# Kernel optimization log

Measured on AMD Instinct MI355X. Metric: run time of the kernel, lower is better.

Reference implementation:

```python
import jax, jax.numpy as jnp
import numpy as np

EPS = 1e-8

def _cosine_rows(a, b):
    na = jnp.maximum(jnp.linalg.norm(a, axis=1), EPS)
    nb = jnp.maximum(jnp.linalg.norm(b, axis=1), EPS)
    return jnp.sum(a * b, axis=1) / (na * nb)


def setup_inputs() -> dict:
    key = jax.random.key(0)
    k1, k2 = jax.random.split(key)
    X = jax.random.normal(k1, (16384, 1024), dtype=jnp.float32)
    dictionary = jax.random.normal(k2, (4096, 1024), dtype=jnp.float32)
    descriptors = jnp.arange(4096, dtype=jnp.int64)
    return {"X": X, "dictionary": dictionary, "descriptors": descriptors, "k": 16}


def reference(X, dictionary, descriptors, k):
    # SOMP with centering=True, criterion='l1', pc=None (default forward path)
    orig_X = X
    std_orig_sum = jnp.sum(jnp.var(orig_X, axis=0, ddof=1))
    X_mean = jnp.mean(X, axis=0, keepdims=True)   # [1, D]
    Xc = X - X_mean                               # centered data [N, D]

    M = dictionary.shape[0]
    notchosen = jnp.ones((M,), dtype=X.dtype)
    residual = Xc
    chosen, evr, l2, cosine = [], [], [], []
    W = None
    recon = jnp.zeros_like(Xc)

    for i in range(k):  # k is a static Python int -> unrolled, per-step shapes static
        cross = residual @ dictionary.T           # [N, M] -- dominant memory traffic
        scores = jnp.sum(jnp.abs(cross * notchosen), axis=0)  # l1 criterion
        idx = jnp.argmax(scores)
        chosen.append(idx)
        notchosen = notchosen.at[idx].set(0)

        atoms = dictionary[jnp.stack(chosen)]     # [i+1, D], dynamic gather, static shape
        # least squares: min ||atoms.T @ W - Xc.T||  (full column rank -> normal eqs)
        G = atoms @ atoms.T                       # [i+1, i+1]
        W = jnp.linalg.solve(G, atoms @ Xc.T)     # [i+1, N]
        recon = (atoms.T @ W).T                   # [N, D]
        residual = Xc - recon

        rec_full = X_mean + recon
        evr.append(jnp.sum(jnp.var(rec_full, axis=0, ddof=1)) / std_orig_sum)
        cosine.append(jnp.mean(_cosine_rows(orig_X, rec_full)))
        l2.append(jnp.mean((orig_X - rec_full) ** 2))

    weights = jnp.linalg.norm(W, axis=1)          # [k]
    chosen_arr = jnp.stack(chosen)
    recon_out = X_mean + recon
    residual_out = Xc - recon                     # == X - recon_out
    return (recon_out, residual_out, chosen_arr, weights, W.T,
            jnp.stack(evr), jnp.stack(l2), jnp.stack(cosine))
```

## Files before the change

### kernel.cpp

```cpp
#include <hip/hip_runtime.h>
#include <math.h>

#define NROWS 16384
#define DIMK  1024
#define MDIC  4096
#define KSEL  16

#define OFF_RECON   0
#define OFF_RESID   ((size_t)NROWS*DIMK)
#define OFF_CHOSEN  ((size_t)2*NROWS*DIMK)
#define OFF_WEIGHTS (OFF_CHOSEN + 16)
#define OFF_WT      (OFF_WEIGHTS + 16)
#define OFF_EVR     (OFF_WT + (size_t)NROWS*KSEL)
#define OFF_L2      (OFF_EVR + 16)
#define OFF_COS     (OFF_L2 + 16)

typedef unsigned short u16;
typedef unsigned long long u64;
typedef __attribute__((ext_vector_type(8))) short short8;
typedef __attribute__((ext_vector_type(4))) float f32x4;

__device__ inline float blockReduce256f(float v) {
    __shared__ float ws_[4];
    #pragma unroll
    for (int off = 32; off > 0; off >>= 1) v += __shfl_down(v, off);
    __syncthreads();
    if ((threadIdx.x & 63) == 0) ws_[threadIdx.x >> 6] = v;
    __syncthreads();
    return ws_[0] + ws_[1] + ws_[2] + ws_[3];
}

__device__ inline void wredStore(double v, int k, int lane, int wv, double (*accS)[4]) {
    #pragma unroll
    for (int off = 32; off > 0; off >>= 1) v += __shfl_down(v, off);
    if (lane == 0) accS[k][wv] = v;
}

__device__ inline u16 f2bf(float f) {
    unsigned u = __float_as_uint(f);
    unsigned r = u + 0x7FFFu + ((u >> 16) & 1u);
    return (u16)(r >> 16);
}
__device__ inline float bf2f(u16 h) { return __uint_as_float(((unsigned)h) << 16); }

__global__ void k_init(float* notchosen, u64* amx, u64* statsAcc, u64* ctr2) {
    int m = blockIdx.x * 256 + threadIdx.x;
    if (m < MDIC) notchosen[m] = 1.0f;
    if (blockIdx.x == 0) {
        if (threadIdx.x < 40) statsAcc[threadIdx.x] = 0ULL;
        if (threadIdx.x < 2)  amx[threadIdx.x] = 0ULL;
        if (threadIdx.x == 0) *ctr2 = 0ULL;
    }
}

__global__ __launch_bounds__(256) void k_colstats(const float* __restrict__ X,
                                                  float* __restrict__ colpart,
                                                  float* __restrict__ sqpart) {
    int d  = blockIdx.x * 256 + threadIdx.x;
    int r0 = blockIdx.y * 256;
    float s = 0.f, sq = 0.f;
    for (int r = 0; r < 256; ++r) {
        float v = X[(size_t)(r0 + r) * DIMK + d];
        s += v; sq += v * v;
    }
    colpart[(size_t)blockIdx.y * DIMK + d] = s;
    __shared__ float red[256];
    red[threadIdx.x] = sq; __syncthreads();
    for (int off = 128; off > 0; off >>= 1) {
        if (threadIdx.x < off) red[threadIdx.x] += red[threadIdx.x + off];
        __syncthreads();
    }
    if (threadIdx.x == 0) sqpart[blockIdx.y * 4 + blockIdx.x] = red[0];
}

__global__ __launch_bounds__(1024) void k_reduce_mean(const float* __restrict__ colpart,
                                                      const float* __restrict__ sqpart,
                                                      float* __restrict__ xmean,
                                                      double* __restrict__ scal) {
    int d = threadIdx.x;
    double s = 0.0;
    for (int y = 0; y < 64; ++y) s += (double)colpart[(size_t)y * DIMK + d];
    float m = (float)(s / (double)NROWS);
    xmean[d] = m;
    __shared__ double red[1024];
    red[d] = (double)m * (double)m; __syncthreads();
    for (int off = 512; off > 0; off >>= 1) {
        if (d < off) red[d] += red[d + off];
        __syncthreads();
    }
    if (d == 0) {
        double xmn2 = red[0];
        double sx2 = 0.0;
        for (int i = 0; i < 256; ++i) sx2 += (double)sqpart[i];
        scal[0] = sx2;
        scal[1] = sx2 - (double)NROWS * xmn2;
        scal[2] = xmn2;
    }
}

__global__ __launch_bounds__(256) void k_md(const float* __restrict__ Dict,
                                            const float* __restrict__ xmean,
                                            float* __restrict__ md,
                                            float* __restrict__ Dnorm2) {
    int m = blockIdx.x, t = threadIdx.x;
    float4 a = ((const float4*)(Dict + (size_t)m * DIMK))[t];
    float4 b = ((const float4*)xmean)[t];
    float s  = a.x * b.x + a.y * b.y + a.z * b.z + a.w * b.w;
    float sn = a.x * a.x + a.y * a.y + a.z * a.z + a.w * a.w;
    s  = blockReduce256f(s);
    sn = blockReduce256f(sn);
    if (t == 0) { md[m] = s; Dnorm2[m] = sn; }
}

__global__ __launch_bounds__(256) void k_split(const float* __restrict__ src,
                                               u16* __restrict__ hi,
                                               u16* __restrict__ lo) {
    size_t idx = ((size_t)blockIdx.x * 256 + threadIdx.x) * 4;
    float4 v = *(const float4*)(src + idx);
    ushort4 h, l;
    h.x = f2bf(v.x); l.x = f2bf(v.x - bf2f(h.x));
    h.y = f2bf(v.y); l.y = f2bf(v.y - bf2f(h.y));
    h.z = f2bf(v.z); l.z = f2bf(v.z - bf2f(h.z));
    h.w = f2bf(v.w); l.w = f2bf(v.w - bf2f(h.w));
    *(ushort4*)(hi + idx) = h;
    *(ushort4*)(lo + idx) = l;
}

__global__ __launch_bounds__(256) void k_splitX(const float* __restrict__ src,
                                                u16* __restrict__ hi,
                                                u16* __restrict__ lo,
                                                const float* __restrict__ xmean,
                                                float* __restrict__ Xnorm2,
                                                float* __restrict__ XdotM) {
    int n = blockIdx.x, t = threadIdx.x;
    size_t idx = (size_t)n * DIMK + t * 4;
    float4 v = *(const float4*)(src + idx);
    float4 mv = ((const float4*)xmean)[t];
    ushort4 h, l;
    h.x = f2bf(v.x); l.x = f2bf(v.x - bf2f(h.x));
    h.y = f2bf(v.y); l.y = f2bf(v.y - bf2f(h.y));
    h.z = f2bf(v.z); l.z = f2bf(v.z - bf2f(h.z));
    h.w = f2bf(v.w); l.w = f2bf(v.w - bf2f(h.w));
    *(ushort4*)(hi + idx) = h;
    *(ushort4*)(lo + idx) = l;
    float s2 = v.x * v.x + v.y * v.y + v.z * v.z + v.w * v.w;
    float sm = v.x * mv.x + v.y * mv.y + v.z * mv.z + v.w * mv.w;
    s2 = blockReduce256f(s2);
    sm = blockReduce256f(sm);
    if (t == 0) { Xnorm2[n] = s2; XdotM[n] = sm; }
}


#define GLL16(g, l) __builtin_amdgcn_global_load_lds( \
    (__attribute__((address_space(1))) void*)(g), \
    (__attribute__((address_space(3))) void*)(l), 16, 0, 0)

#define STAGE_A2(pa_, kc_, wb_, q0_, q1_) do { \
    GLL16((pa_) + aGbase + (size_t)(q0_) * 64 * DIMK + (kc_), \
          sA + (wb_) * 16384 + (q0_) * 4096 + lWbase); \
    GLL16((pa_) + aGbase + (size_t)(q1_) * 64 * DIMK + (kc_), \
          sA + (wb_) * 16384 + (q1_) * 4096 + lWbase); \
} while (0)

#define STAGE_B2(pb_, kc_, wb_, q0_, q1_) do { \
    GLL16((pb_) + bGbase + (size_t)(q0_) * 64 * DIMK + (kc_), \
          sB + (wb_) * 16384 + (q0_) * 4096 + lWbase); \
    GLL16((pb_) + bGbase + (size_t)(q1_) * 64 * DIMK + (kc_), \
          sB + (wb_) * 16384 + (q1_) * 4096 + lWbase); \
} while (0)

#define VM4 asm volatile("s_waitcnt vmcnt(4)" ::: "memory")
#define VM2 asm volatile("s_waitcnt vmcnt(2)" ::: "memory")
#define VM0 asm volatile("s_waitcnt vmcnt(0)" ::: "memory")
#define NOPSTMT ((void)0)

#define PHASE(rb_, mq_, nq_, STAGE_STMT, WAIT_STMT) do { \
    short8 af[4][2], bfv[2][2]; \
    const u16* pA_ = sA + (rb_) * 16384; \
    const u16* pB_ = sB + (rb_) * 16384; \
    _Pragma("unroll") \
    for (int fi = 0; fi < 4; ++fi) { \
        af[fi][0] = *(const short8*)&pA_[aoffA0 + ((mq_) * 4 + fi) * 1024]; \
        af[fi][1] = *(const short8*)&pA_[aoffA1 + ((mq_) * 4 + fi) * 1024]; \
    } \
    _Pragma("unroll") \
    for (int fj = 0; fj < 2; ++fj) { \
        bfv[fj][0] = *(const short8*)&pB_[boffB0 + ((nq_) * 2 + fj) * 1024]; \
        bfv[fj][1] = *(const short8*)&pB_[boffB1 + ((nq_) * 2 + fj) * 1024]; \
    } \
    STAGE_STMT; \
    __builtin_amdgcn_s_barrier(); \
    __builtin_amdgcn_s_setprio(1); \
    _Pragma("unroll") \
    for (int fi = 0; fi < 4; ++fi) \
        _Pragma("unroll") \
        for (int fj = 0; fj < 2; ++fj) { \
            acc[(mq_) * 4 + fi][(nq_) * 2 + fj] = __builtin_amdgcn_mfma_f32_16x16x32_bf16( \
                af[fi][0], bfv[fj][0], acc[(mq_) * 4 + fi][(nq_) * 2 + fj], 0, 0, 0); \
            acc[(mq_) * 4 + fi][(nq_) * 2 + fj] = __builtin_amdgcn_mfma_f32_16x16x32_bf16( \
                af[fi][1], bfv[fj][1], acc[(mq_) * 4 + fi][(nq_) * 2 + fj], 0, 0, 0); \
        } \
    __builtin_amdgcn_s_setprio(0); \
    WAIT_STMT; \
    __builtin_amdgcn_s_barrier(); \
} while (0)

__global__ __launch_bounds__(512, 2) void k_gemm8(const u16* __restrict__ Ahi,
                                                  const u16* __restrict__ Alo,
                                                  const u16* __restrict__ Bhi,
                                                  const u16* __restrict__ Blo,
                                                  const float* __restrict__ md,
                                                  u16* __restrict__ C0h,
                                                  int rowAbase) {
    __shared__ u16 sA[2 * 16384];
    __shared__ u16 sB[2 * 16384];
    int T = threadIdx.x;
    int lane = T & 63, wid = T >> 6;
    int wr = wid >> 2, wc = wid & 3;

    int nwg = gridDim.x, cpx = nwg >> 3;
    int bid = blockIdx.x;
    int wg  = (bid & 7) * cpx + (bid >> 3);
    int bm = wg >> 4, bn = wg & 15;
    int rowA0 = bm * 256, rowB0 = bn * 256;

    int sw = (T & 7) ^ ((T >> 3) & 7);
    size_t aGbase = (size_t)(rowA0 + (T >> 3)) * DIMK + sw * 8;
    size_t bGbase = (size_t)(rowB0 + (T >> 3)) * DIMK + sw * 8;
    int lWbase = (T >> 6) * 512;

    int lm = lane & 15, lk = lane >> 4;
    int kb0 = (lk * 16) ^ ((lane & 7) << 4);
    int kb1 = (64 + lk * 16) ^ ((lane & 7) << 4);
    int aoffA0 = (wr * 128 + lm) * 64 + (kb0 >> 1);
    int aoffA1 = (wr * 128 + lm) * 64 + (kb1 >> 1);
    int boffB0 = (wc * 64 + lm) * 64 + (kb0 >> 1);
    int boffB1 = (wc * 64 + lm) * 64 + (kb1 >> 1);

    f32x4 acc[8][4];
    f32x4 zero = {0.f, 0.f, 0.f, 0.f};
    #pragma unroll
    for (int i = 0; i < 8; ++i)
        #pragma unroll
        for (int j = 0; j < 4; ++j) acc[i][j] = zero;

    STAGE_B2(Bhi, 0, 0, 0, 1);
    STAGE_B2(Bhi, 0, 0, 2, 3);
    STAGE_A2(Ahi, 0, 0, 0, 2);
    STAGE_A2(Ahi, 0, 0, 1, 3);
    VM2;
    __builtin_amdgcn_s_barrier();

    for (int t = 0; t < 47; ++t) {
        int rbuf = t & 1, wbuf = rbuf ^ 1;
        int kk = (t + 1) << 6;
        int seg = kk >> 10;
        const u16* pa = (seg == 1) ? Alo : Ahi;
        const u16* pb = (seg == 2) ? Blo : Bhi;
        int kc = kk & 1023;
        PHASE(rbuf, 0, 0, STAGE_B2(pb, kc, wbuf, 0, 1), NOPSTMT);
        PHASE(rbuf, 0, 1, STAGE_B2(pb, kc, wbuf, 2, 3), VM4);
        PHASE(rbuf, 1, 0, STAGE_A2(pa, kc, wbuf, 0, 2), NOPSTMT);
        PHASE(rbuf, 1, 1, STAGE_A2(pa, kc, wbuf, 1, 3), VM2);
    }
    PHASE(1, 0, 0, NOPSTMT, NOPSTMT);
    PHASE(1, 0, 1, NOPSTMT, VM0);
    PHASE(1, 1, 0, NOPSTMT, NOPSTMT);
    PHASE(1, 1, 1, NOPSTMT, NOPSTMT);

    #pragma unroll
    for (int nf = 0; nf < 4; ++nf) {
        int m = rowB0 + wc * 64 + nf * 16 + lm;
        float mdv = md[m];
        #pragma unroll
        for (int mf = 0; mf < 8; ++mf) {
            int nb = rowAbase + rowA0 + wr * 128 + mf * 16 + lk * 4;
            #pragma unroll
            for (int r = 0; r < 4; ++r)
                C0h[(size_t)(nb + r) * MDIC + m] = f2bf(acc[mf][nf][r] - mdv);
        }
    }
}

template <int NA>
__global__ __launch_bounds__(256) void k_score(const u16* __restrict__ C0h,
                                               const float* __restrict__ GR,
                                               const float* __restrict__ Wm,
                                               float* __restrict__ scorePf) {
    constexpr int NAX = NA ? NA : 1;
    __shared__ float Wl[NAX][64];
    int t = threadIdx.x;
    int m0 = blockIdx.x * 1024 + t * 4;
    int n0 = blockIdx.y * 64;
    float4 gr[NAX];
    #pragma unroll
    for (int j = 0; j < NA; ++j) gr[j] = *(const float4*)&GR[(size_t)j * MDIC + m0];
    for (int idx = t; idx < NA * 64; idx += 256) {
        int j = idx >> 6, nn = idx & 63;
        Wl[j][nn] = Wm[(size_t)j * NROWS + n0 + nn];
    }
    __syncthreads();
    float4 acc = {0.f, 0.f, 0.f, 0.f};
    for (int nn = 0; nn < 64; ++nn) {
        ushort4 ch = *(const ushort4*)&C0h[(size_t)(n0 + nn) * MDIC + m0];
        float4 c = {bf2f(ch.x), bf2f(ch.y), bf2f(ch.z), bf2f(ch.w)};
        float4 cr = {0.f, 0.f, 0.f, 0.f};
        #pragma unroll
        for (int j = 0; j < NA; ++j) {
            float wv = Wl[j][nn];
            cr.x += wv * gr[j].x; cr.y += wv * gr[j].y;
            cr.z += wv * gr[j].z; cr.w += wv * gr[j].w;
        }
        acc.x += fabsf(c.x - cr.x); acc.y += fabsf(c.y - cr.y);
        acc.z += fabsf(c.z - cr.z); acc.w += fabsf(c.w - cr.w);
    }
    *(float4*)&scorePf[(size_t)blockIdx.y * MDIC + m0] = acc;
}

__global__ __launch_bounds__(256) void k_scoreargmax(const float* __restrict__ scorePf,
                                                     float* __restrict__ notchosen,
                                                     u64* __restrict__ amx,
                                                     int* __restrict__ chosen,
                                                     float* __restrict__ outChosen,
                                                     const float* __restrict__ md,
                                                     const float* __restrict__ Dnorm2,
                                                     const float* __restrict__ GR,
                                                     float* __restrict__ Lmat,
                                                     float* __restrict__ Gcc,
                                                     float* __restrict__ mdot,
                                                     int iter) {
    int t = threadIdx.x;
    int m0 = blockIdx.x * 256;
    int tm = t & 63, yg = t >> 6;
    float sx = 0.f, sy = 0.f, sz = 0.f, sw = 0.f;
    #pragma unroll 4
    for (int y = yg; y < 256; y += 4) {
        float4 v = *(const float4*)&scorePf[(size_t)y * MDIC + m0 + (tm << 2)];
        sx += v.x; sy += v.y; sz += v.z; sw += v.w;
    }
    __shared__ float4 red4[4][64];
    float4 pv; pv.x = sx; pv.y = sy; pv.z = sz; pv.w = sw;
    red4[yg][tm] = pv;
    __syncthreads();
    u64 best = 0ULL;
    if (t < 64) {
        float4 a = red4[0][t], b = red4[1][t], cc = red4[2][t], d = red4[3][t];
        double sv[4] = {(double)a.x + b.x + cc.x + d.x,
                        (double)a.y + b.y + cc.y + d.y,
                        (double)a.z + b.z + cc.z + d.z,
                        (double)a.w + b.w + cc.w + d.w};
        int mb = m0 + (t << 2);
        #pragma unroll
        for (int j = 0; j < 4; ++j) {
            if (notchosen[mb + j] != 0.f) {
                u64 key = ((u64)__double_as_longlong(sv[j]) & ~0xFFFULL) | (u64)(4095 - (mb + j));
                if (key > best) best = key;
            }
        }
        #pragma unroll
        for (int off = 32; off > 0; off >>= 1) {
            u64 o = __shfl_down(best, off);
            if (o > best) best = o;
        }
    }
    __shared__ int slast, sc;
    if (t == 0) {
        atomicMax(&amx[0], best);
        __threadfence();
        u64 done = atomicAdd(&amx[1], 1ULL);
        slast = (done == 15ULL) ? 1 : 0;
        if (slast) {
            u64 k = atomicMax(&amx[0], 0ULL);
            int c = 4095 - (int)(k & 0xFFFULL);
            sc = c;
            chosen[iter] = c;
            notchosen[c] = 0.f;
            outChosen[iter] = (float)c;
            mdot[iter] = md[c];
            amx[0] = 0ULL; amx[1] = 0ULL;
        }
    }
    __syncthreads();
    if (!slast) return;
    int c = sc;
    __shared__ float Lsh[16][16];
    __shared__ float g[17];
    __shared__ float LrowS[16];
    Lsh[t >> 4][t & 15] = Lmat[t];
    if (t < iter)  g[t] = GR[(size_t)t * MDIC + c];
    if (t == iter) g[t] = Dnorm2[c];
    __syncthreads();
    if (t == 0) {
        for (int b = 0; b < iter; ++b) {
            float s = g[b];
            for (int x = 0; x < b; ++x) s -= LrowS[x] * Lsh[b][x];
            LrowS[b] = s / Lsh[b][b];
        }
        float s2 = g[iter];
        for (int x = 0; x < iter; ++x) s2 -= LrowS[x] * LrowS[x];
        LrowS[iter] = sqrtf(fmaxf(s2, 1e-20f));
        for (int b = 0; b <= iter; ++b) Lmat[iter * 16 + b] = LrowS[b];
        for (int b = iter + 1; b < 16; ++b) Lmat[iter * 16 + b] = 0.f;
        for (int b = 0; b < iter; ++b) { Gcc[iter * 16 + b] = g[b]; Gcc[b * 16 + iter] = g[b]; }
        Gcc[iter * 16 + iter] = g[iter];
    }
}

template <int NAT>
__global__ __launch_bounds__(256) void k_gramsolve(const float* __restrict__ Dict,
                                                   const int* __restrict__ chosen,
                                                   const u16* __restrict__ C0h,
                                                   float* __restrict__ GR,
                                                   float* __restrict__ Bm,
                                                   const float* __restrict__ Lmat,
                                                   const float* __restrict__ Gcc_g,
                                                   const float* __restrict__ mdot,
                                                   const float* __restrict__ Xnorm2,
                                                   const float* __restrict__ XdotM,
                                                   const double* __restrict__ scal,
                                                   float* __restrict__ Wm,
                                                   u64* __restrict__ statsAcc,
                                                   u64* __restrict__ ctr2,
                                                   float* __restrict__ out, int iter) {
    int t = threadIdx.x;
    int c = chosen[iter];
    if (blockIdx.x >= 64) {
        int m = blockIdx.x - 64;
        float4 a = ((const float4*)(Dict + (size_t)c * DIMK))[t];
        float4 b = ((const float4*)(Dict + (size_t)m * DIMK))[t];
        float s = a.x * b.x + a.y * b.y + a.z * b.z + a.w * b.w;
        s = blockReduce256f(s);
        if (t == 0) GR[(size_t)iter * MDIC + m] = s;
        return;
    }
    constexpr int NV = 3 + 2 * NAT;
    __shared__ float L[16][16];
    __shared__ float G[16][16];
    __shared__ float mdl[16];
    __shared__ double accS[35][4];
    if (t < NAT * NAT) {
        int a = t / NAT, b2 = t % NAT;
        L[a][b2] = Lmat[a * 16 + b2];
        G[a][b2] = Gcc_g[a * 16 + b2];
    }
    if (t < NAT) mdl[t] = mdot[t];
    __syncthreads();
    int n = blockIdx.x * 256 + t;
    float b[NAT], y[NAT], w[NAT];
    #pragma unroll
    for (int j = 0; j < NAT - 1; ++j) b[j] = Bm[(size_t)j * NROWS + n];
    float bn = bf2f(C0h[(size_t)n * MDIC + c]);
    b[NAT - 1] = bn;
    Bm[(size_t)(NAT - 1) * NROWS + n] = bn;
    #pragma unroll
    for (int a = 0; a < NAT; ++a) {
        float s = b[a];
        #pragma unroll
        for (int x = 0; x < NAT; ++x) if (x < a) s -= L[a][x] * y[x];
        y[a] = s / L[a][a];
    }
    #pragma unroll
    for (int a = NAT - 1; a >= 0; --a) {
        float s = y[a];
        #pragma unroll
        for (int x = 0; x < NAT; ++x) if (x > a) s -= L[x][a] * w[x];
        w[a] = s / L[a][a];
    }
    #pragma unroll
    for (int j = 0; j < NAT; ++j) Wm[(size_t)j * NROWS + n] = w[j];

    float q = 0.f, wb = 0.f, wmd = 0.f, num1 = 0.f;
    #pragma unroll
    for (int j = 0; j < NAT; ++j) {
        float gw = 0.f;
        #pragma unroll
        for (int x = 0; x < NAT; ++x) gw += G[j][x] * w[x];
        q    += w[j] * gw;
        wb   += w[j] * b[j];
        wmd  += w[j] * mdl[j];
        num1 += w[j] * (b[j] + mdl[j]);
    }
    float xmn2 = (float)scal[2];
    float rec2 = xmn2 + 2.f * wmd + q;
    float na = fmaxf(sqrtf(Xnorm2[n]), 1e-8f);
    float nb = fmaxf(sqrtf(fmaxf(rec2, 0.f)), 1e-8f);
    float cosn = (XdotM[n] + num1) / (na * nb);

    int lane = t & 63, wv = t >> 6;
    wredStore((double)q,    0, lane, wv, accS);
    wredStore((double)wb,   1, lane, wv, accS);
    wredStore((double)cosn, 2, lane, wv, accS);
    #pragma unroll
    for (int j = 0; j < NAT; ++j) {
        wredStore((double)w[j],                 3 + j,       lane, wv, accS);
        wredStore((double)w[j] * (double)w[j],  3 + NAT + j, lane, wv, accS);
    }
    __syncthreads();
    if (t < NV) {
        double tot = accS[t][0] + accS[t][1] + accS[t][2] + accS[t][3];
        long long fx = (long long)(tot * 1048576.0);
        atomicAdd(&statsAcc[t], (u64)fx);
    }
    __shared__ int slast2;
    __syncthreads();
    if (t == 0) {
        __threadfence();
        slast2 = (atomicAdd(ctr2, 1ULL) == 63ULL) ? 1 : 0;
    }
    __syncthreads();
    if (!slast2) return;
    __shared__ double stot[35];
    __shared__ double wbarS[16];
    if (t < NV) {
        u64 raw = atomicAdd(&statsAcc[t], 0ULL);
        stot[t] = (double)(long long)raw * (1.0 / 1048576.0);
        statsAcc[t] = 0ULL;
    }
    if (t == 0) *ctr2 = 0ULL;
    __syncthreads();
    if (t < NAT) wbarS[t] = stot[3 + t] * (1.0 / (double)NROWS);
    __syncthreads();
    if (t == 0) {
        double q2 = stot[0], wb2 = stot[1], cs = stot[2];
        double wg = 0.0;
        for (int a = 0; a < NAT; ++a)
            for (int b2 = 0; b2 < NAT; ++b2) wg += wbarS[a] * wbarS[b2] * (double)G[a][b2];
        double sumXc2 = scal[1];
        out[OFF_EVR + iter] = (float)((q2 - (double)NROWS * wg) / sumXc2);
        out[OFF_L2  + iter] = (float)((sumXc2 - 2.0 * wb2 + q2) / ((double)NROWS * (double)DIMK));
        out[OFF_COS + iter] = (float)(cs / (double)NROWS);
        if (NAT == KSEL) {
            for (int j = 0; j < NAT; ++j)
                out[OFF_WEIGHTS + j] = (float)sqrt(stot[3 + NAT + j]);
        }
    }
}

__global__ __launch_bounds__(256) void k_outfinal(const float* __restrict__ X,
                                                  const float* __restrict__ xmean,
                                                  const float* __restrict__ Dict,
                                                  const int* __restrict__ chosen,
                                                  const float* __restrict__ Wm,
                                                  float* __restrict__ out) {
    __shared__ int cI[16];
    int t = threadIdx.x;
    if (t < 16) cI[t] = chosen[t];
    __syncthreads();
    int n0 = blockIdx.x * 8;
    if (t < 128) {
        int j = t & 15, r = t >> 4;
        int n = n0 + r;
        out[OFF_WT + (size_t)n * 16 + j] = Wm[(size_t)j * NROWS + n];
    }
    float4 xm = ((const float4*)xmean)[t];
    for (int r = 0; r < 8; ++r) {
        int n = n0 + r;
        float w[16];
        #pragma unroll
        for (int j = 0; j < 16; ++j) w[j] = Wm[(size_t)j * NROWS + n];
        float4 rec = xm;
        #pragma unroll
        for (int j = 0; j < 16; ++j) {
            float4 a = ((const float4*)(Dict + (size_t)cI[j] * DIMK))[t];
            rec.x += w[j] * a.x; rec.y += w[j] * a.y;
            rec.z += w[j] * a.z; rec.w += w[j] * a.w;
        }
        float4 xv = ((const float4*)(X + (size_t)n * DIMK))[t];
        float4 res = {xv.x - rec.x, xv.y - rec.y, xv.z - rec.z, xv.w - rec.w};
        ((float4*)(out + OFF_RECON + (size_t)n * DIMK))[t] = rec;
        ((float4*)(out + OFF_RESID + (size_t)n * DIMK))[t] = res;
    }
}

struct IterArgs {
    const float *X, *Dict;
    u16 *C0h;
    float *GR, *W, *Bm, *md, *Dnorm2, *xmean, *Xnorm2, *XdotM, *notchosen, *Lmat, *Gcc, *mdot;
    float *scorePf;
    u64 *amx, *statsAcc, *ctr2;
    double *scal;
    int *chosen;
    float *out;
    hipStream_t stream;
};

template <int I>
static void run_iter(const IterArgs& a) {
    k_score<I><<<dim3(4, 256), 256, 0, a.stream>>>(a.C0h, a.GR, a.W, a.scorePf);
    k_scoreargmax<<<16, 256, 0, a.stream>>>(a.scorePf, a.notchosen, a.amx, a.chosen,
                                            a.out + OFF_CHOSEN, a.md, a.Dnorm2, a.GR,
                                            a.Lmat, a.Gcc, a.mdot, I);
    k_gramsolve<I + 1><<<MDIC + 64, 256, 0, a.stream>>>(a.Dict, a.chosen, a.C0h, a.GR,
                                                        a.Bm, a.Lmat, a.Gcc, a.mdot,
                                                        a.Xnorm2, a.XdotM, a.scal, a.W,
                                                        a.statsAcc, a.ctr2, a.out, I);
}

template <int I>
struct Loop {
    static void go(const IterArgs& a) { run_iter<I>(a); Loop<I + 1>::go(a); }
};
template <>
struct Loop<KSEL> { static void go(const IterArgs&) {} };

extern "C" void kernel_launch(void* const* d_in, const int* in_sizes, int n_in,
                              void* d_out, int out_size, void* d_ws, size_t ws_size,
                              hipStream_t stream) {
    (void)in_sizes; (void)n_in; (void)out_size;
    const float* X    = (const float*)d_in[0];
    const float* Dict = (const float*)d_in[1];
    float* out = (float*)d_out;

    char* ws = (char*)d_ws;
    size_t off = 0;
    auto carve = [&](size_t bytes) -> char* {
        char* p = ws + off;
        off += (bytes + 255) & ~(size_t)255;
        return p;
    };
    u16*    C0h       = (u16*)   carve((size_t)NROWS * MDIC * 2);
    float*  GR        = (float*) carve((size_t)KSEL * MDIC * 4);
    float*  W         = (float*) carve((size_t)KSEL * NROWS * 4);
    float*  Bm        = (float*) carve((size_t)KSEL * NROWS * 4);
    float*  md        = (float*) carve((size_t)MDIC * 4);
    float*  Dnorm2    = (float*) carve((size_t)MDIC * 4);
    float*  xmean     = (float*) carve((size_t)DIMK * 4);
    float*  colpart   = (float*) carve((size_t)64 * DIMK * 4);
    float*  sqpart    = (float*) carve(256 * 4);
    float*  Xnorm2    = (float*) carve((size_t)NROWS * 4);
    float*  XdotM     = (float*) carve((size_t)NROWS * 4);
    float*  scorePf   = (float*) carve((size_t)256 * MDIC * 4);
    float*  notchosen = (float*) carve((size_t)MDIC * 4);
    u64*    amx       = (u64*)   carve(2 * 8);
    u64*    statsAcc  = (u64*)   carve(40 * 8);
    u64*    ctr2      = (u64*)   carve(8);
    int*    chosen    = (int*)   carve(KSEL * 4);
    float*  Lmat      = (float*) carve(256 * 4);
    float*  Gcc       = (float*) carve(256 * 4);
    float*  mdot      = (float*) carve(16 * 4);
    double* scal      = (double*)carve(8 * 8);
    u16*    Bhi       = (u16*)   carve((size_t)MDIC * DIMK * 2);
    u16*    Blo       = (u16*)   carve((size_t)MDIC * DIMK * 2);

    int chunkrows = 0;
    for (int cr = NROWS; cr >= 256; cr >>= 1) {
        size_t need = (size_t)cr * DIMK * 2 * 2 + 512;
        if (off + need <= ws_size) { chunkrows = cr; break; }
    }
    if (chunkrows == 0) chunkrows = 256;
    u16* Ahi = (u16*) carve((size_t)chunkrows * DIMK * 2);
    u16* Alo = (u16*) carve((size_t)chunkrows * DIMK * 2);

    k_init<<<MDIC / 256, 256, 0, stream>>>(notchosen, amx, statsAcc, ctr2);
    k_colstats<<<dim3(4, 64), 256, 0, stream>>>(X, colpart, sqpart);
    k_reduce_mean<<<1, 1024, 0, stream>>>(colpart, sqpart, xmean, scal);
    k_md<<<MDIC, 256, 0, stream>>>(Dict, xmean, md, Dnorm2);

    k_split<<<(MDIC * DIMK) / 1024, 256, 0, stream>>>(Dict, Bhi, Blo);
    int nchunks = NROWS / chunkrows;
    for (int c = 0; c < nchunks; ++c) {
        k_splitX<<<chunkrows, 256, 0, stream>>>(
            X + (size_t)c * chunkrows * DIMK, Ahi, Alo, xmean,
            Xnorm2 + (size_t)c * chunkrows, XdotM + (size_t)c * chunkrows);
        int mtiles = chunkrows / 256;
        k_gemm8<<<dim3(mtiles * 16), 512, 0, stream>>>(
            Ahi, Alo, Bhi, Blo, md, C0h, c * chunkrows);
    }

    IterArgs a{X, Dict, C0h, GR, W, Bm, md, Dnorm2, xmean, Xnorm2, XdotM, notchosen,
               Lmat, Gcc, mdot, scorePf, amx, statsAcc, ctr2, scal, chosen, out, stream};
    Loop<0>::go(a);

    k_outfinal<<<NROWS / 8, 256, 0, stream>>>(X, xmean, Dict, chosen, W, out);
}
```

Measured before the change: 1.524 ms.

## Reorder GEMM inner phases by k-half to reuse B fragments across phases

The four per-tile phases of the bf16 MFMA GEMM are reorganised. Each phase now covers one k-half for a 4x4 block of accumulators instead of a 4x2 block over the full k slice. B fragments loaded in the first phase of each k-half are kept in registers and reused by the next phase, which loads only A. This halves the LDS fragment reads per tile. The global-load wait moves from the second phase to the first, which may expose more memory latency, and the extra live fragment registers could raise register pressure.

```diff
diff --git a/kernel.cpp b/kernel.cpp
--- a/kernel.cpp
+++ b/kernel.cpp
@@ -169,37 +169,49 @@
           sB + (wb_) * 16384 + (q1_) * 4096 + lWbase); \
 } while (0)
 
-#define VM4 asm volatile("s_waitcnt vmcnt(4)" ::: "memory")
 #define VM2 asm volatile("s_waitcnt vmcnt(2)" ::: "memory")
 #define VM0 asm volatile("s_waitcnt vmcnt(0)" ::: "memory")
 #define NOPSTMT ((void)0)
 
-#define PHASE(rb_, mq_, nq_, STAGE_STMT, WAIT_STMT) do { \
-    short8 af[4][2], bfv[2][2]; \
+#define PHASE_BA(rb_, s_, STAGE_STMT, WAIT_STMT) do { \
     const u16* pA_ = sA + (rb_) * 16384; \
     const u16* pB_ = sB + (rb_) * 16384; \
+    int ko_ = (s_) ? koff1 : koff0; \
     _Pragma("unroll") \
-    for (int fi = 0; fi < 4; ++fi) { \
-        af[fi][0] = *(const short8*)&pA_[aoffA0 + ((mq_) * 4 + fi) * 1024]; \
-        af[fi][1] = *(const short8*)&pA_[aoffA1 + ((mq_) * 4 + fi) * 1024]; \
-    } \
+    for (int nf = 0; nf < 4; ++nf) \
+        bq[nf] = *(const short8*)&pB_[boffB + nf * 1024 + ko_]; \
     _Pragma("unroll") \
-    for (int fj = 0; fj < 2; ++fj) { \
-        bfv[fj][0] = *(const short8*)&pB_[boffB0 + ((nq_) * 2 + fj) * 1024]; \
-        bfv[fj][1] = *(const short8*)&pB_[boffB1 + ((nq_) * 2 + fj) * 1024]; \
-    } \
+    for (int fi = 0; fi < 4; ++fi) \
+        aq[fi] = *(const short8*)&pA_[aoffA + fi * 1024 + ko_]; \
     STAGE_STMT; \
     __builtin_amdgcn_s_barrier(); \
     __builtin_amdgcn_s_setprio(1); \
     _Pragma("unroll") \
     for (int fi = 0; fi < 4; ++fi) \
         _Pragma("unroll") \
-        for (int fj = 0; fj < 2; ++fj) { \
-            acc[(mq_) * 4 + fi][(nq_) * 2 + fj] = __builtin_amdgcn_mfma_f32_16x16x32_bf16( \
-                af[fi][0], bfv[fj][0], acc[(mq_) * 4 + fi][(nq_) * 2 + fj], 0, 0, 0); \
-            acc[(mq_) * 4 + fi][(nq_) * 2 + fj] = __builtin_amdgcn_mfma_f32_16x16x32_bf16( \
-                af[fi][1], bfv[fj][1], acc[(mq_) * 4 + fi][(nq_) * 2 + fj], 0, 0, 0); \
-        } \
+        for (int nf = 0; nf < 4; ++nf) \
+            acc[fi][nf] = __builtin_amdgcn_mfma_f32_16x16x32_bf16( \
+                aq[fi], bq[nf], acc[fi][nf], 0, 0, 0); \
+    __builtin_amdgcn_s_setprio(0); \
+    WAIT_STMT; \
+    __builtin_amdgcn_s_barrier(); \
+} while (0)
+
+#define PHASE_A(rb_, s_, STAGE_STMT, WAIT_STMT) do { \
+    const u16* pA_ = sA + (rb_) * 16384; \
+    int ko_ = (s_) ? koff1 : koff0; \
+    _Pragma("unroll") \
+    for (int fi = 0; fi < 4; ++fi) \
+        aq[fi] = *(const short8*)&pA_[aoffA + (4 + fi) * 1024 + ko_]; \
+    STAGE_STMT; \
+    __builtin_amdgcn_s_barrier(); \
+    __builtin_amdgcn_s_setprio(1); \
+    _Pragma("unroll") \
+    for (int fi = 0; fi < 4; ++fi) \
+        _Pragma("unroll") \
+        for (int nf = 0; nf < 4; ++nf) \
+            acc[4 + fi][nf] = __builtin_amdgcn_mfma_f32_16x16x32_bf16( \
+                aq[fi], bq[nf], acc[4 + fi][nf], 0, 0, 0); \
     __builtin_amdgcn_s_setprio(0); \
     WAIT_STMT; \
     __builtin_amdgcn_s_barrier(); \
@@ -232,10 +244,9 @@
     int lm = lane & 15, lk = lane >> 4;
     int kb0 = (lk * 16) ^ ((lane & 7) << 4);
     int kb1 = (64 + lk * 16) ^ ((lane & 7) << 4);
-    int aoffA0 = (wr * 128 + lm) * 64 + (kb0 >> 1);
-    int aoffA1 = (wr * 128 + lm) * 64 + (kb1 >> 1);
-    int boffB0 = (wc * 64 + lm) * 64 + (kb0 >> 1);
-    int boffB1 = (wc * 64 + lm) * 64 + (kb1 >> 1);
+    int koff0 = kb0 >> 1, koff1 = kb1 >> 1;
+    int aoffA = (wr * 128 + lm) * 64;
+    int boffB = (wc * 64 + lm) * 64;
 
     f32x4 acc[8][4];
     f32x4 zero = {0.f, 0.f, 0.f, 0.f};
@@ -243,6 +254,7 @@
     for (int i = 0; i < 8; ++i)
         #pragma unroll
         for (int j = 0; j < 4; ++j) acc[i][j] = zero;
+    short8 bq[4], aq[4];
 
     STAGE_B2(Bhi, 0, 0, 0, 1);
     STAGE_B2(Bhi, 0, 0, 2, 3);
@@ -258,15 +270,15 @@
         const u16* pa = (seg == 1) ? Alo : Ahi;
         const u16* pb = (seg == 2) ? Blo : Bhi;
         int kc = kk & 1023;
-        PHASE(rbuf, 0, 0, STAGE_B2(pb, kc, wbuf, 0, 1), NOPSTMT);
-        PHASE(rbuf, 0, 1, STAGE_B2(pb, kc, wbuf, 2, 3), VM4);
-        PHASE(rbuf, 1, 0, STAGE_A2(pa, kc, wbuf, 0, 2), NOPSTMT);
-        PHASE(rbuf, 1, 1, STAGE_A2(pa, kc, wbuf, 1, 3), VM2);
-    }
-    PHASE(1, 0, 0, NOPSTMT, NOPSTMT);
-    PHASE(1, 0, 1, NOPSTMT, VM0);
-    PHASE(1, 1, 0, NOPSTMT, NOPSTMT);
-    PHASE(1, 1, 1, NOPSTMT, NOPSTMT);
+        PHASE_BA(rbuf, 0, STAGE_B2(pb, kc, wbuf, 0, 1), VM2);
+        PHASE_A (rbuf, 0, STAGE_B2(pb, kc, wbuf, 2, 3), NOPSTMT);
+        PHASE_BA(rbuf, 1, STAGE_A2(pa, kc, wbuf, 0, 2), NOPSTMT);
+        PHASE_A (rbuf, 1, STAGE_A2(pa, kc, wbuf, 1, 3), VM2);
+    }
+    PHASE_BA(1, 0, NOPSTMT, VM0);
+    PHASE_A (1, 0, NOPSTMT, NOPSTMT);
+    PHASE_BA(1, 1, NOPSTMT, NOPSTMT);
+    PHASE_A (1, 1, NOPSTMT, NOPSTMT);
 
     #pragma unroll
     for (int nf = 0; nf < 4; ++nf) {
```

Result: faster. 1.476 ms (-3.2%).
